# Kernel tuning notes

Hardware: AMD Instinct MI355X
Metric: run time of the kernel (lower is better)

## Reference

```python
import jax, jax.numpy as jnp
import numpy as np

N_NODES = 50000
N_EDGES = 600000
IN_CH, HID, EMB = 128, 128, 64


def _glorot(key, shape):
    fan_in, fan_out = shape[1], shape[0]
    lim = np.sqrt(6.0 / (fan_in + fan_out))
    return jax.random.uniform(key, shape, jnp.float32, -lim, lim)


def setup_inputs() -> dict:
    key = jax.random.key(0)
    ks = jax.random.split(key, 12)
    x = jax.random.normal(ks[0], (N_NODES, IN_CH), jnp.float32)
    edge_index = jax.random.randint(ks[1], (2, N_EDGES), 0, N_NODES, jnp.int64)
    return {
        "x": x,
        "edge_index": edge_index,
        # SAGEConv layer 1: lin_l (neighbor, with bias) + lin_r (root, no bias)
        "w1n": _glorot(ks[2], (HID, IN_CH)),
        "w1r": _glorot(ks[3], (HID, IN_CH)),
        "b1": jnp.zeros((HID,), jnp.float32),
        "w2n": _glorot(ks[4], (HID, HID)),
        "w2r": _glorot(ks[5], (HID, HID)),
        "b2": jnp.zeros((HID,), jnp.float32),
        "w3n": _glorot(ks[6], (EMB, HID)),
        "w3r": _glorot(ks[7], (EMB, HID)),
        "b3": jnp.zeros((EMB,), jnp.float32),
    }


def _sage_conv(x, src, dst, wn, wr, b):
    # mean aggregation of source-node features at destination nodes
    msg = x[src]                                            # [E, d_in]
    agg = jax.ops.segment_sum(msg, dst, num_segments=N_NODES)
    deg = jax.ops.segment_sum(jnp.ones((src.shape[0],), x.dtype), dst,
                              num_segments=N_NODES)
    agg = agg / jnp.maximum(deg, 1.0)[:, None]
    return agg @ wn.T + x @ wr.T + b


def reference(x, edge_index, w1n, w1r, b1, w2n, w2r, b2, w3n, w3r, b3):
    src, dst = edge_index[0], edge_index[1]
    h = jax.nn.relu(_sage_conv(x, src, dst, w1n, w1r, b1))
    # dropout(p=0.3) is identity in inference mode
    h = jax.nn.relu(_sage_conv(h, src, dst, w2n, w2r, b2))
    h = _sage_conv(h, src, dst, w3n, w3r, b3)
    return h
```

## Files before the change

### kernel.cpp

```cpp
#include <hip/hip_runtime.h>
#include <hip/hip_bf16.h>

#define NN 50000
#define ELLW 64
#define F8MINDEG 6

#define NB 128
#define BSH 9
#define BCAP 8192
#define EPB 2048

typedef short bf16x8 __attribute__((ext_vector_type(8)));
typedef float f32x4 __attribute__((ext_vector_type(4)));
typedef float floatx2 __attribute__((ext_vector_type(2)));

#if __has_builtin(__builtin_amdgcn_cvt_pk_f32_fp8) && __has_builtin(__builtin_amdgcn_cvt_pk_fp8_f32)
#define HWF8 1
#endif

__device__ __forceinline__ float bf_lo(unsigned int p) {
    union { unsigned int u; float f; } c; c.u = p << 16; return c.f;
}
__device__ __forceinline__ float bf_hi(unsigned int p) {
    union { unsigned int u; float f; } c; c.u = p & 0xffff0000u; return c.f;
}
__device__ __forceinline__ unsigned short bfbits(float f) {
    __hip_bfloat16 h = __float2bfloat16(f);
    union { __hip_bfloat16 b; unsigned short s; } c; c.b = h; return c.s;
}
__device__ __forceinline__ unsigned int pack_bf(float a, float b) {
    return (unsigned int)bfbits(a) | ((unsigned int)bfbits(b) << 16);
}
__device__ __forceinline__ void stv(float* p, float v) { *p = v; }
__device__ __forceinline__ void stv(unsigned short* p, float v) { *p = bfbits(v); }

__device__ __forceinline__ floatx2 bfpair(unsigned int p) {
    union { unsigned int u; float f; } lo, hi;
    lo.u = p << 16; hi.u = p & 0xffff0000u;
    return floatx2{lo.f, hi.f};
}
__device__ __forceinline__ void acc8v(const uint4& u, floatx2* a) {
    a[0] += bfpair(u.x); a[1] += bfpair(u.y);
    a[2] += bfpair(u.z); a[3] += bfpair(u.w);
}

__device__ __forceinline__ unsigned int enc1(float f) {
#ifdef HWF8
    return (unsigned int)__builtin_amdgcn_cvt_pk_fp8_f32(f, f, 0, false) & 0xffu;
#else
    union { float f; unsigned u; } c; c.f = f;
    unsigned s = (c.u >> 24) & 0x80u;
    float af = fabsf(f);
    if (af >= 448.f) return s | 0x7eu;
    if (af < 0.0078125f) {
        unsigned m = (unsigned)(af * 512.f + 0.5f);
        return s | (m > 7u ? 7u : m);
    }
    unsigned u = c.u & 0x7fffffffu;
    u += 0x7ffffu + ((u >> 20) & 1u);
    int e = (int)(u >> 23) - 120;
    if (e < 1) { unsigned m = (unsigned)(af * 512.f + 0.5f); return s | (m > 7u ? 7u : m); }
    if (e > 15) return s | 0x7eu;
    return s | ((unsigned)e << 3) | ((u >> 20) & 7u);
#endif
}
__device__ __forceinline__ unsigned int packf8_4(float x, float y, float z, float w) {
#ifdef HWF8
    int u = __builtin_amdgcn_cvt_pk_fp8_f32(x, y, 0, false);
    u = __builtin_amdgcn_cvt_pk_fp8_f32(z, w, u, true);
    return (unsigned int)u;
#else
    return enc1(x) | (enc1(y) << 8) | (enc1(z) << 16) | (enc1(w) << 24);
#endif
}
__device__ __forceinline__ void accf8v(const uint4& u, floatx2* a) {
#ifdef HWF8
    a[0] += __builtin_amdgcn_cvt_pk_f32_fp8(u.x, false);
    a[1] += __builtin_amdgcn_cvt_pk_f32_fp8(u.x, true);
    a[2] += __builtin_amdgcn_cvt_pk_f32_fp8(u.y, false);
    a[3] += __builtin_amdgcn_cvt_pk_f32_fp8(u.y, true);
    a[4] += __builtin_amdgcn_cvt_pk_f32_fp8(u.z, false);
    a[5] += __builtin_amdgcn_cvt_pk_f32_fp8(u.z, true);
    a[6] += __builtin_amdgcn_cvt_pk_f32_fp8(u.w, false);
    a[7] += __builtin_amdgcn_cvt_pk_f32_fp8(u.w, true);
#else
    const unsigned ww[4] = {u.x, u.y, u.z, u.w};
#pragma unroll
    for (int k = 0; k < 4; k++) {
#pragma unroll
        for (int j = 0; j < 4; j++) {
            unsigned b = (ww[k] >> (8 * j)) & 0xffu;
            unsigned v = ((b & 0x80u) << 24) | (((b & 0x7fu) + (120u << 3)) << 20);
            if ((b & 0x78u) == 0) v = 0u;
            union { unsigned u; float f; } c; c.u = v;
            a[(k * 4 + j) >> 1][(k * 4 + j) & 1] += c.f;
        }
    }
#endif
}

__global__ __launch_bounds__(256) void wb3z_kernel(
    const float* __restrict__ w1n, const float* __restrict__ w1r,
    const float* __restrict__ w2n, const float* __restrict__ w2r,
    const float* __restrict__ w3n, const float* __restrict__ w3r,
    unsigned short* __restrict__ wB1, unsigned short* __restrict__ wB2,
    unsigned short* __restrict__ wB3, unsigned int* __restrict__ bpos) {
    int i = blockIdx.x * blockDim.x + threadIdx.x;
    if (i < NB) bpos[i] = 0u;
    if (i >= 12288) return;
    if (i < 8192) {
        const float* wn = (i < 4096) ? w1n : w2n;
        const float* wr = (i < 4096) ? w1r : w2r;
        unsigned short* wB = (i < 4096) ? wB1 : wB2;
        int li = i & 4095;
        int row = li >> 5;
        int j = (li & 31) * 4;
        float4 a = *(const float4*)(wn + (size_t)row * 128 + j);
        float4 b = *(const float4*)(wr + (size_t)row * 128 + j);
        *(uint2*)(wB + (size_t)row * 256 + j) = uint2{pack_bf(a.x, a.y), pack_bf(a.z, a.w)};
        *(uint2*)(wB + (size_t)row * 256 + 128 + j) = uint2{pack_bf(b.x, b.y), pack_bf(b.z, b.w)};
    } else {
        int li = i - 8192;
        const float* w = (li < 2048) ? w3n : w3r;
        int rbase = (li < 2048) ? 0 : 64;
        int lj = li & 2047;
        int row = lj >> 5;
        int j = (lj & 31) * 4;
        float4 a = *(const float4*)(w + (size_t)row * 128 + j);
        *(uint2*)(wB3 + (size_t)(rbase + row) * 128 + j) =
            uint2{pack_bf(a.x, a.y), pack_bf(a.z, a.w)};
    }
}

__global__ __launch_bounds__(256) void binify_cvt_kernel(
    const float* __restrict__ x,
    unsigned short* __restrict__ xb,
    unsigned char* __restrict__ xf8,
    const int* __restrict__ src,
    const int* __restrict__ dst,
    unsigned int* __restrict__ bpos,
    unsigned int* __restrict__ barr,
    int n4, int E, int nEB) {
    __shared__ int cnt[NB];
    __shared__ int gbase[NB];
    const int t = threadIdx.x;
    const int blk = blockIdx.x;
    if (blk < nEB) {
        int e0 = blk * EPB;
        int ss[8], dd[8], rr[8];
        bool v[8];
#pragma unroll
        for (int k = 0; k < 8; k++) {
            int e = e0 + t + (k << 8);
            v[k] = (e < E);
            ss[k] = v[k] ? src[e] : 0;
            dd[k] = v[k] ? dst[e] : 0;
            rr[k] = 0;
        }
        if (t < NB) cnt[t] = 0;
        __syncthreads();
#pragma unroll
        for (int k = 0; k < 8; k++)
            if (v[k]) rr[k] = atomicAdd(&cnt[dd[k] >> BSH], 1);
        __syncthreads();
        if (t < NB) {
            int c = cnt[t];
            gbase[t] = c ? (int)atomicAdd(&bpos[t], (unsigned)c) : 0;
        }
        __syncthreads();
#pragma unroll
        for (int k = 0; k < 8; k++) {
            if (v[k]) {
                int b = dd[k] >> BSH;
                int pos = gbase[b] + rr[k];
                if (pos < BCAP)
                    barr[b * BCAP + pos] =
                        (unsigned)ss[k] | ((unsigned)dd[k] << 16);
            }
        }
    }
    int gtid = blk * 256 + t;
    int gs = gridDim.x << 8;
    for (int i = gtid; i < n4; i += gs) {
        float4 vv = *(const float4*)(x + 4 * (size_t)i);
        *(uint2*)(xb + 4 * (size_t)i) = uint2{pack_bf(vv.x, vv.y), pack_bf(vv.z, vv.w)};
        *(unsigned int*)(xf8 + 4 * (size_t)i) = packf8_4(vv.x, vv.y, vv.z, vv.w);
    }
}

__global__ __launch_bounds__(256) void ellbuild_kernel(
    const unsigned int* __restrict__ bpos,
    const unsigned int* __restrict__ barr,
    unsigned short* __restrict__ ell,
    int* __restrict__ cnt) {
    __shared__ alignas(16) unsigned short lell[512 * 64];
    __shared__ int lcnt[512];
    const int t = threadIdx.x;
    const int b = blockIdx.x;
    for (int i = t; i < 4096; i += 256) ((uint4*)lell)[i] = uint4{0u, 0u, 0u, 0u};
    for (int i = t; i < 512; i += 256) lcnt[i] = 0;
    __syncthreads();
    int ne = (int)bpos[b];
    if (ne > BCAP) ne = BCAP;
    const unsigned int* seg = barr + (size_t)b * BCAP;
    for (int i = t; i < ne; i += 256) {
        unsigned p = seg[i];
        int ln = (p >> 16) & 511;
        int r = atomicAdd(&lcnt[ln], 1);
        lell[(ln << 6) + (r & (ELLW - 1))] = (unsigned short)(p & 0xffffu);
    }
    __syncthreads();
    int node0 = b << BSH;
    int nn = NN - node0;
    if (nn > 512) nn = 512;
    if (nn <= 0) return;
    uint4* gell = (uint4*)(ell + (size_t)node0 * ELLW);
    const uint4* sell = (const uint4*)lell;
    for (int i = t; i < nn * 8; i += 256) gell[i] = sell[i];
    for (int i = t; i < nn; i += 256) cnt[node0 + i] = lcnt[i];
}

__global__ __launch_bounds__(256) void gather_kernel(
    const int* __restrict__ cnt, const unsigned short* __restrict__ ell,
    const unsigned char* __restrict__ hf8,
    const unsigned short* __restrict__ hb,
    unsigned short* __restrict__ axc,
    int n_nodes) {
    int tid = blockIdx.x * blockDim.x + threadIdx.x;
    int n = tid >> 3;
    if (n >= n_nodes) return;
    int c = (tid & 7) << 4;
    int deg = cnt[n];
    int dd = min(deg, ELLW);
    const unsigned short* cl = ell + (size_t)n * ELLW;
    floatx2 a[8];
#pragma unroll
    for (int k = 0; k < 8; k++) a[k] = floatx2{0.f, 0.f};
    if (deg >= F8MINDEG) {
        int i = 0;
        for (; i + 7 < dd; i += 8) {
            uint4 idv = *(const uint4*)(cl + i);
            int i0 = idv.x & 0xffff, i1 = idv.x >> 16;
            int i2 = idv.y & 0xffff, i3 = idv.y >> 16;
            int i4 = idv.z & 0xffff, i5 = idv.z >> 16;
            int i6 = idv.w & 0xffff, i7 = idv.w >> 16;
            uint4 u0 = *(const uint4*)(hf8 + (size_t)i0 * 128 + c);
            uint4 u1 = *(const uint4*)(hf8 + (size_t)i1 * 128 + c);
            uint4 u2 = *(const uint4*)(hf8 + (size_t)i2 * 128 + c);
            uint4 u3 = *(const uint4*)(hf8 + (size_t)i3 * 128 + c);
            uint4 u4 = *(const uint4*)(hf8 + (size_t)i4 * 128 + c);
            uint4 u5 = *(const uint4*)(hf8 + (size_t)i5 * 128 + c);
            uint4 u6 = *(const uint4*)(hf8 + (size_t)i6 * 128 + c);
            uint4 u7 = *(const uint4*)(hf8 + (size_t)i7 * 128 + c);
            accf8v(u0, a); accf8v(u1, a); accf8v(u2, a); accf8v(u3, a);
            accf8v(u4, a); accf8v(u5, a); accf8v(u6, a); accf8v(u7, a);
        }
        for (; i < dd; i++) {
            uint4 u = *(const uint4*)(hf8 + (size_t)cl[i] * 128 + c);
            accf8v(u, a);
        }
    } else {
        for (int i = 0; i < dd; i++) {
            int s = cl[i];
            uint4 lo = *(const uint4*)(hb + (size_t)s * 128 + c);
            uint4 hi = *(const uint4*)(hb + (size_t)s * 128 + c + 8);
            acc8v(lo, a); acc8v(hi, a + 4);
        }
    }
    float s = 1.0f / (float)max(deg, 1);
    uint4 p0 = {pack_bf(a[0][0] * s, a[0][1] * s), pack_bf(a[1][0] * s, a[1][1] * s),
                pack_bf(a[2][0] * s, a[2][1] * s), pack_bf(a[3][0] * s, a[3][1] * s)};
    uint4 p1 = {pack_bf(a[4][0] * s, a[4][1] * s), pack_bf(a[5][0] * s, a[5][1] * s),
                pack_bf(a[6][0] * s, a[6][1] * s), pack_bf(a[7][0] * s, a[7][1] * s)};
    *(uint4*)(axc + (size_t)n * 128 + c) = p0;
    *(uint4*)(axc + (size_t)n * 128 + c + 8) = p1;
}

__global__ __launch_bounds__(256) void gather_add_kernel(
    const int* __restrict__ cnt, const unsigned short* __restrict__ ell,
    const unsigned short* __restrict__ tu,
    const float* __restrict__ b3,
    float* __restrict__ out, int n_nodes) {
    int tid = blockIdx.x * blockDim.x + threadIdx.x;
    int n = tid >> 3;
    if (n >= n_nodes) return;
    int c = (tid & 7) << 3;
    int deg = cnt[n];
    int dd = min(deg, ELLW);
    const unsigned short* cl = ell + (size_t)n * ELLW;
    floatx2 a[4];
#pragma unroll
    for (int k = 0; k < 4; k++) a[k] = floatx2{0.f, 0.f};
    int i = 0;
    for (; i + 7 < dd; i += 8) {
        uint4 idv = *(const uint4*)(cl + i);
        int i0 = idv.x & 0xffff, i1 = idv.x >> 16;
        int i2 = idv.y & 0xffff, i3 = idv.y >> 16;
        int i4 = idv.z & 0xffff, i5 = idv.z >> 16;
        int i6 = idv.w & 0xffff, i7 = idv.w >> 16;
        uint4 u0 = *(const uint4*)(tu + (size_t)i0 * 128 + c);
        uint4 u1 = *(const uint4*)(tu + (size_t)i1 * 128 + c);
        uint4 u2 = *(const uint4*)(tu + (size_t)i2 * 128 + c);
        uint4 u3 = *(const uint4*)(tu + (size_t)i3 * 128 + c);
        uint4 u4 = *(const uint4*)(tu + (size_t)i4 * 128 + c);
        uint4 u5 = *(const uint4*)(tu + (size_t)i5 * 128 + c);
        uint4 u6 = *(const uint4*)(tu + (size_t)i6 * 128 + c);
        uint4 u7 = *(const uint4*)(tu + (size_t)i7 * 128 + c);
        acc8v(u0, a); acc8v(u1, a); acc8v(u2, a); acc8v(u3, a);
        acc8v(u4, a); acc8v(u5, a); acc8v(u6, a); acc8v(u7, a);
    }
    for (; i < dd; i++) {
        uint4 u = *(const uint4*)(tu + (size_t)cl[i] * 128 + c);
        acc8v(u, a);
    }
    float s = 1.0f / (float)max(deg, 1);
    uint4 uu = *(const uint4*)(tu + (size_t)n * 128 + 64 + c);
    float4 bA = *(const float4*)(b3 + c);
    float4 bB = *(const float4*)(b3 + c + 4);
    float* o = out + (size_t)n * 64 + c;
    o[0] = a[0][0] * s + bf_lo(uu.x) + bA.x;
    o[1] = a[0][1] * s + bf_hi(uu.x) + bA.y;
    o[2] = a[1][0] * s + bf_lo(uu.y) + bA.z;
    o[3] = a[1][1] * s + bf_hi(uu.y) + bA.w;
    o[4] = a[2][0] * s + bf_lo(uu.z) + bB.x;
    o[5] = a[2][1] * s + bf_hi(uu.z) + bB.y;
    o[6] = a[3][0] * s + bf_lo(uu.w) + bB.z;
    o[7] = a[3][1] * s + bf_hi(uu.w) + bB.w;
}

template <int NKS, bool RELU, bool BIAS, bool F8, typename OUT_T>
__global__ __launch_bounds__(256) void mfma_gemm(
    const unsigned short* __restrict__ A0, const unsigned short* __restrict__ A1,
    const unsigned short* __restrict__ B,
    const float* __restrict__ bias,
    OUT_T* __restrict__ out, unsigned char* __restrict__ f8out,
    int M, int N, int nTilesN) {
    constexpr int KTOT = NKS * 64;
    constexpr int LDB = KTOT + 8;
    __shared__ unsigned short As[2][128 * 72];
    __shared__ unsigned short Bs[64 * LDB];
    const int t = threadIdx.x;
    const int w = t >> 6, l = t & 63;
    const int tileM = blockIdx.x / nTilesN;
    const int n0 = (blockIdx.x - tileM * nTilesN) * 64;
    const int m0 = tileM * 128;
    const int lr = l & 15, lq = l >> 4;

    for (int c = t; c < 64 * (KTOT / 8); c += 256) {
        int row = c / (KTOT / 8);
        int ko = (c - row * (KTOT / 8)) * 8;
        *(uint4*)(&Bs[row * LDB + ko]) =
            *(const uint4*)(&B[(size_t)(n0 + row) * KTOT + ko]);
    }
    for (int c = t; c < 1024; c += 256) {
        int row = c >> 3;
        int ko = (c & 7) * 8;
        int gm = m0 + row;
        uint4 v = {0u, 0u, 0u, 0u};
        if (gm < M) v = *(const uint4*)(A0 + (size_t)gm * 128 + ko);
        *(uint4*)(&As[0][row * 72 + ko]) = v;
    }
    __syncthreads();

    f32x4 acc[2][4];
#pragma unroll
    for (int tm = 0; tm < 2; tm++)
#pragma unroll
        for (int tn = 0; tn < 4; tn++) acc[tm][tn] = f32x4{0.f, 0.f, 0.f, 0.f};

#pragma unroll
    for (int ks = 0; ks < NKS; ks++) {
        uint4 pf[4];
        if (ks + 1 < NKS) {
            int ns = ks + 1;
            const unsigned short* Asrc = (ns < NKS / 2)
                ? (A0 + (size_t)ns * 64) : (A1 + (size_t)(ns - NKS / 2) * 64);
#pragma unroll
            for (int j = 0; j < 4; j++) {
                int c = t + j * 256;
                int row = c >> 3;
                int ko = (c & 7) * 8;
                int gm = m0 + row;
                pf[j] = uint4{0u, 0u, 0u, 0u};
                if (gm < M) pf[j] = *(const uint4*)(Asrc + (size_t)gm * 128 + ko);
            }
        }
        const unsigned short* as = As[ks & 1];
#pragma unroll
        for (int kc = 0; kc < 2; kc++) {
            int lk = kc * 32 + lq * 8;
            bf16x8 af[2], bfr[4];
            af[0] = *(const bf16x8*)(&as[(w * 32 + lr) * 72 + lk]);
            af[1] = *(const bf16x8*)(&as[(w * 32 + 16 + lr) * 72 + lk]);
#pragma unroll
            for (int tn = 0; tn < 4; tn++)
                bfr[tn] = *(const bf16x8*)(&Bs[(tn * 16 + lr) * LDB + ks * 64 + lk]);
#pragma unroll
            for (int tm = 0; tm < 2; tm++)
#pragma unroll
                for (int tn = 0; tn < 4; tn++)
                    acc[tm][tn] = __builtin_amdgcn_mfma_f32_16x16x32_bf16(
                        af[tm], bfr[tn], acc[tm][tn], 0, 0, 0);
        }
        if (ks + 1 < NKS) {
#pragma unroll
            for (int j = 0; j < 4; j++) {
                int c = t + j * 256;
                int row = c >> 3;
                int ko = (c & 7) * 8;
                *(uint4*)(&As[(ks + 1) & 1][row * 72 + ko]) = pf[j];
            }
            __syncthreads();
        }
    }

#pragma unroll
    for (int tn = 0; tn < 4; tn++) {
        int n = n0 + tn * 16 + lr;
        float bj = BIAS ? bias[n] : 0.f;
#pragma unroll
        for (int tm = 0; tm < 2; tm++) {
#pragma unroll
            for (int i = 0; i < 4; i++) {
                int m = m0 + w * 32 + tm * 16 + lq * 4 + i;
                if (m < M) {
                    float v = acc[tm][tn][i] + bj;
                    if (RELU) v = fmaxf(v, 0.f);
                    stv(&out[(size_t)m * N + n], v);
                    if (F8) f8out[(size_t)m * N + n] = (unsigned char)enc1(v);
                }
            }
        }
    }
}

extern "C" void kernel_launch(void* const* d_in, const int* in_sizes, int n_in,
                              void* d_out, int out_size, void* d_ws, size_t ws_size,
                              hipStream_t stream) {
    const float* x  = (const float*)d_in[0];
    const int* ei   = (const int*)d_in[1];
    const float* w1n = (const float*)d_in[2];
    const float* w1r = (const float*)d_in[3];
    const float* b1  = (const float*)d_in[4];
    const float* w2n = (const float*)d_in[5];
    const float* w2r = (const float*)d_in[6];
    const float* b2  = (const float*)d_in[7];
    const float* w3n = (const float*)d_in[8];
    const float* w3r = (const float*)d_in[9];
    const float* b3  = (const float*)d_in[10];
    float* out = (float*)d_out;

    const int E = in_sizes[1] / 2;
    const int* src = ei;
    const int* dst = ei + E;

    char* ws = (char*)d_ws;
    unsigned short* xb  = (unsigned short*)(ws);
    unsigned short* axc = (unsigned short*)(ws + 12800000);
    unsigned short* h1b = (unsigned short*)(ws + 25600000);
    unsigned short* h2b = (unsigned short*)(ws + 38400000);
    unsigned int* barr  = (unsigned int*)(ws + 38400000);
    int* cnt            = (int*)  (ws + 51200000);
    unsigned int* bpos  = (unsigned int*)(ws + 51400192);
    unsigned short* ell = (unsigned short*)(ws + 54400000);
    unsigned short* wB1 = (unsigned short*)(ws + 60800000);
    unsigned short* wB2 = (unsigned short*)(ws + 60865536);
    unsigned short* wB3 = (unsigned short*)(ws + 60931072);
    unsigned char* xf8  = (unsigned char*)(ws + 60963840);
    unsigned char* h1f8 = (unsigned char*)(ws + 67363840);

    const int nEB = (E + EPB - 1) / EPB;

    wb3z_kernel<<<48, 256, 0, stream>>>(
        w1n, w1r, w2n, w2r, w3n, w3r, wB1, wB2, wB3, bpos);
    binify_cvt_kernel<<<2048, 256, 0, stream>>>(x, xb, xf8, src, dst,
                                                bpos, barr, NN * 32, E, nEB);
    ellbuild_kernel<<<(NN + 511) / 512, 256, 0, stream>>>(bpos, barr, ell, cnt);

    const int gatherBlocks = (NN * 8 + 255) / 256;
    const int mTiles = (NN + 127) / 128;

    gather_kernel<<<gatherBlocks, 256, 0, stream>>>(cnt, ell, xf8, xb, axc, NN);
    mfma_gemm<4, true, true, true, unsigned short>
        <<<mTiles * 2, 256, 0, stream>>>(axc, xb, wB1, b1, h1b, h1f8, NN, 128, 2);

    gather_kernel<<<gatherBlocks, 256, 0, stream>>>(cnt, ell, h1f8, h1b, axc, NN);
    mfma_gemm<4, true, true, false, unsigned short>
        <<<mTiles * 2, 256, 0, stream>>>(axc, h1b, wB2, b2, h2b, nullptr, NN, 128, 2);

    mfma_gemm<2, false, false, false, unsigned short>
        <<<mTiles * 2, 256, 0, stream>>>(h2b, h2b + 64, wB3, nullptr, axc, nullptr,
                                         NN, 128, 2);
    gather_add_kernel<<<gatherBlocks, 256, 0, stream>>>(
        cnt, ell, axc, b3, out, NN);
}
```

Measured before the change: 233.5 us.

## Sort nodes by degree and pad ELL rows with zero-row sentinel

Builds a degree histogram in the ELL build, prefix-sums it, and scatters nodes into a degree-sorted ELL copy with a permutation. The gathers then iterate in that sorted order, so neighbouring threads have similar degrees and wavefront divergence drops. ELL padding now points at a zeroed sentinel row, which removes the scalar tail loops and lets every iteration fetch eight neighbours at once. This adds two small kernels and an extra pass that copies the ELL, and it spends bandwidth loading padding entries.

Result: slower. 337.4 us (+44.5%).

```diff
diff --git a/kernel.cpp b/kernel.cpp
--- a/kernel.cpp
+++ b/kernel.cpp
@@ -2,6 +2,7 @@
 #include <hip/hip_bf16.h>
 
 #define NN 50000
+#define ZROW 50000
 #define ELLW 64
 #define F8MINDEG 6
 
@@ -104,9 +105,20 @@
     const float* __restrict__ w2n, const float* __restrict__ w2r,
     const float* __restrict__ w3n, const float* __restrict__ w3r,
     unsigned short* __restrict__ wB1, unsigned short* __restrict__ wB2,
-    unsigned short* __restrict__ wB3, unsigned int* __restrict__ bpos) {
+    unsigned short* __restrict__ wB3, int* __restrict__ zblk,
+    unsigned short* __restrict__ xb, unsigned short* __restrict__ axc,
+    unsigned short* __restrict__ h1b,
+    unsigned char* __restrict__ xf8, unsigned char* __restrict__ h1f8) {
     int i = blockIdx.x * blockDim.x + threadIdx.x;
-    if (i < NB) bpos[i] = 0u;
+    if (i < 2048) zblk[i] = 0;
+    int p = i - 2048;
+    if (p >= 0 && p < 256) {
+        if (p < 64)       ((unsigned int*)(xb  + (size_t)ZROW * 128))[p] = 0u;
+        else if (p < 128) ((unsigned int*)(axc + (size_t)ZROW * 128))[p - 64] = 0u;
+        else if (p < 192) ((unsigned int*)(h1b + (size_t)ZROW * 128))[p - 128] = 0u;
+        else if (p < 224) ((unsigned int*)(xf8 + (size_t)ZROW * 128))[p - 192] = 0u;
+        else              ((unsigned int*)(h1f8 + (size_t)ZROW * 128))[p - 224] = 0u;
+    }
     if (i >= 12288) return;
     if (i < 8192) {
         const float* wn = (i < 4096) ? w1n : w2n;
@@ -192,13 +204,17 @@
     const unsigned int* __restrict__ bpos,
     const unsigned int* __restrict__ barr,
     unsigned short* __restrict__ ell,
-    int* __restrict__ cnt) {
+    int* __restrict__ cnt,
+    int* __restrict__ hist) {
     __shared__ alignas(16) unsigned short lell[512 * 64];
     __shared__ int lcnt[512];
+    __shared__ int lh[65];
     const int t = threadIdx.x;
     const int b = blockIdx.x;
-    for (int i = t; i < 4096; i += 256) ((uint4*)lell)[i] = uint4{0u, 0u, 0u, 0u};
+    const unsigned PADP = 0xC350C350u;
+    for (int i = t; i < 4096; i += 256) ((uint4*)lell)[i] = uint4{PADP, PADP, PADP, PADP};
     for (int i = t; i < 512; i += 256) lcnt[i] = 0;
+    if (t < 65) lh[t] = 0;
     __syncthreads();
     int ne = (int)bpos[b];
     if (ne > BCAP) ne = BCAP;
@@ -217,28 +233,60 @@
     uint4* gell = (uint4*)(ell + (size_t)node0 * ELLW);
     const uint4* sell = (const uint4*)lell;
     for (int i = t; i < nn * 8; i += 256) gell[i] = sell[i];
-    for (int i = t; i < nn; i += 256) cnt[node0 + i] = lcnt[i];
+    for (int i = t; i < nn; i += 256) {
+        int d = lcnt[i];
+        cnt[node0 + i] = d;
+        atomicAdd(&lh[min(d, 64)], 1);
+    }
+    __syncthreads();
+    if (t < 65 && lh[t]) atomicAdd(&hist[t], lh[t]);
+}
+
+__global__ void prefix65_kernel(const int* __restrict__ hist, int* __restrict__ cursor) {
+    if (threadIdx.x == 0) {
+        int r = 0;
+        for (int d = 0; d <= 64; d++) { cursor[d * 16] = r; r += hist[d]; }
+    }
+}
+
+__global__ __launch_bounds__(256) void place_kernel(
+    const int* __restrict__ cnt, int* __restrict__ cursor,
+    const unsigned short* __restrict__ ell,
+    unsigned short* __restrict__ ell2,
+    int* __restrict__ perm, int* __restrict__ degS) {
+    int tid = blockIdx.x * blockDim.x + threadIdx.x;
+    int n = tid >> 3, ln = tid & 7;
+    if (n >= NN) return;
+    int deg = cnt[n];
+    int pos = 0;
+    if (ln == 0) pos = atomicAdd(&cursor[min(deg, 64) * 16], 1);
+    int lane = threadIdx.x & 63;
+    pos = __shfl(pos, lane & 56, 64);
+    ((uint4*)(ell2 + (size_t)pos * ELLW))[ln] =
+        ((const uint4*)(ell + (size_t)n * ELLW))[ln];
+    if (ln == 0) { perm[pos] = n; degS[pos] = deg; }
 }
 
 __global__ __launch_bounds__(256) void gather_kernel(
-    const int* __restrict__ cnt, const unsigned short* __restrict__ ell,
+    const int* __restrict__ degS, const int* __restrict__ perm,
+    const unsigned short* __restrict__ ell2,
     const unsigned char* __restrict__ hf8,
     const unsigned short* __restrict__ hb,
     unsigned short* __restrict__ axc,
     int n_nodes) {
     int tid = blockIdx.x * blockDim.x + threadIdx.x;
-    int n = tid >> 3;
-    if (n >= n_nodes) return;
+    int j = tid >> 3;
+    if (j >= n_nodes) return;
     int c = (tid & 7) << 4;
-    int deg = cnt[n];
-    int dd = min(deg, ELLW);
-    const unsigned short* cl = ell + (size_t)n * ELLW;
+    int deg = degS[j];
+    int n = perm[j];
+    int dd8 = (min(deg, ELLW) + 7) & ~7;
+    const unsigned short* cl = ell2 + (size_t)j * ELLW;
     floatx2 a[8];
 #pragma unroll
     for (int k = 0; k < 8; k++) a[k] = floatx2{0.f, 0.f};
     if (deg >= F8MINDEG) {
-        int i = 0;
-        for (; i + 7 < dd; i += 8) {
+        for (int i = 0; i < dd8; i += 8) {
             uint4 idv = *(const uint4*)(cl + i);
             int i0 = idv.x & 0xffff, i1 = idv.x >> 16;
             int i2 = idv.y & 0xffff, i3 = idv.y >> 16;
@@ -255,16 +303,20 @@
             accf8v(u0, a); accf8v(u1, a); accf8v(u2, a); accf8v(u3, a);
             accf8v(u4, a); accf8v(u5, a); accf8v(u6, a); accf8v(u7, a);
         }
-        for (; i < dd; i++) {
-            uint4 u = *(const uint4*)(hf8 + (size_t)cl[i] * 128 + c);
-            accf8v(u, a);
-        }
     } else {
-        for (int i = 0; i < dd; i++) {
-            int s = cl[i];
-            uint4 lo = *(const uint4*)(hb + (size_t)s * 128 + c);
-            uint4 hi = *(const uint4*)(hb + (size_t)s * 128 + c + 8);
-            acc8v(lo, a); acc8v(hi, a + 4);
+        for (int i = 0; i < dd8; i += 8) {
+            uint4 idv = *(const uint4*)(cl + i);
+            int is[8];
+            is[0] = idv.x & 0xffff; is[1] = idv.x >> 16;
+            is[2] = idv.y & 0xffff; is[3] = idv.y >> 16;
+            is[4] = idv.z & 0xffff; is[5] = idv.z >> 16;
+            is[6] = idv.w & 0xffff; is[7] = idv.w >> 16;
+#pragma unroll
+            for (int k = 0; k < 8; k++) {
+                uint4 lo = *(const uint4*)(hb + (size_t)is[k] * 128 + c);
+                uint4 hi = *(const uint4*)(hb + (size_t)is[k] * 128 + c + 8);
+                acc8v(lo, a); acc8v(hi, a + 4);
+            }
         }
     }
     float s = 1.0f / (float)max(deg, 1);
@@ -277,22 +329,23 @@
 }
 
 __global__ __launch_bounds__(256) void gather_add_kernel(
-    const int* __restrict__ cnt, const unsigned short* __restrict__ ell,
+    const int* __restrict__ degS, const int* __restrict__ perm,
+    const unsigned short* __restrict__ ell2,
     const unsigned short* __restrict__ tu,
     const float* __restrict__ b3,
     float* __restrict__ out, int n_nodes) {
     int tid = blockIdx.x * blockDim.x + threadIdx.x;
-    int n = tid >> 3;
-    if (n >= n_nodes) return;
+    int j = tid >> 3;
+    if (j >= n_nodes) return;
     int c = (tid & 7) << 3;
-    int deg = cnt[n];
-    int dd = min(deg, ELLW);
-    const unsigned short* cl = ell + (size_t)n * ELLW;
+    int deg = degS[j];
+    int n = perm[j];
+    int dd8 = (min(deg, ELLW) + 7) & ~7;
+    const unsigned short* cl = ell2 + (size_t)j * ELLW;
     floatx2 a[4];
 #pragma unroll
     for (int k = 0; k < 4; k++) a[k] = floatx2{0.f, 0.f};
-    int i = 0;
-    for (; i + 7 < dd; i += 8) {
+    for (int i = 0; i < dd8; i += 8) {
         uint4 idv = *(const uint4*)(cl + i);
         int i0 = idv.x & 0xffff, i1 = idv.x >> 16;
         int i2 = idv.y & 0xffff, i3 = idv.y >> 16;
@@ -308,10 +361,6 @@
         uint4 u7 = *(const uint4*)(tu + (size_t)i7 * 128 + c);
         acc8v(u0, a); acc8v(u1, a); acc8v(u2, a); acc8v(u3, a);
         acc8v(u4, a); acc8v(u5, a); acc8v(u6, a); acc8v(u7, a);
-    }
-    for (; i < dd; i++) {
-        uint4 u = *(const uint4*)(tu + (size_t)cl[i] * 128 + c);
-        acc8v(u, a);
     }
     float s = 1.0f / (float)max(deg, 1);
     uint4 uu = *(const uint4*)(tu + (size_t)n * 128 + 64 + c);
@@ -456,35 +505,44 @@
 
     char* ws = (char*)d_ws;
     unsigned short* xb  = (unsigned short*)(ws);
-    unsigned short* axc = (unsigned short*)(ws + 12800000);
-    unsigned short* h1b = (unsigned short*)(ws + 25600000);
-    unsigned short* h2b = (unsigned short*)(ws + 38400000);
-    unsigned int* barr  = (unsigned int*)(ws + 38400000);
-    int* cnt            = (int*)  (ws + 51200000);
-    unsigned int* bpos  = (unsigned int*)(ws + 51400192);
-    unsigned short* ell = (unsigned short*)(ws + 54400000);
-    unsigned short* wB1 = (unsigned short*)(ws + 60800000);
-    unsigned short* wB2 = (unsigned short*)(ws + 60865536);
-    unsigned short* wB3 = (unsigned short*)(ws + 60931072);
-    unsigned char* xf8  = (unsigned char*)(ws + 60963840);
-    unsigned char* h1f8 = (unsigned char*)(ws + 67363840);
+    unsigned short* axc = (unsigned short*)(ws + 13000000);
+    unsigned short* h1b = (unsigned short*)(ws + 26000000);
+    unsigned short* h2b = (unsigned short*)(ws + 39000000);
+    unsigned int* barr  = (unsigned int*)(ws + 39000000);
+    unsigned short* ell = (unsigned short*)(ws + 52000000);
+    unsigned short* ell2= (unsigned short*)(ws + 58400000);
+    int* cnt            = (int*)  (ws + 64800000);
+    int* perm           = (int*)  (ws + 65000000);
+    int* degS           = (int*)  (ws + 65200000);
+    int* zblk           = (int*)  (ws + 65400000);
+    int* hist           = zblk;
+    int* cursor         = zblk + 256;
+    unsigned int* bpos  = (unsigned int*)(zblk + 1536);
+    unsigned short* wB1 = (unsigned short*)(ws + 65500000);
+    unsigned short* wB2 = (unsigned short*)(ws + 65600000);
+    unsigned short* wB3 = (unsigned short*)(ws + 65700000);
+    unsigned char* xf8  = (unsigned char*)(ws + 65800000);
+    unsigned char* h1f8 = (unsigned char*)(ws + 72300000);
 
     const int nEB = (E + EPB - 1) / EPB;
 
     wb3z_kernel<<<48, 256, 0, stream>>>(
-        w1n, w1r, w2n, w2r, w3n, w3r, wB1, wB2, wB3, bpos);
+        w1n, w1r, w2n, w2r, w3n, w3r, wB1, wB2, wB3, zblk, xb, axc, h1b, xf8, h1f8);
     binify_cvt_kernel<<<2048, 256, 0, stream>>>(x, xb, xf8, src, dst,
                                                 bpos, barr, NN * 32, E, nEB);
-    ellbuild_kernel<<<(NN + 511) / 512, 256, 0, stream>>>(bpos, barr, ell, cnt);
+    ellbuild_kernel<<<(NN + 511) / 512, 256, 0, stream>>>(bpos, barr, ell, cnt, hist);
+    prefix65_kernel<<<1, 64, 0, stream>>>(hist, cursor);
+    place_kernel<<<(NN * 8 + 255) / 256, 256, 0, stream>>>(cnt, cursor, ell, ell2,
+                                                           perm, degS);
 
     const int gatherBlocks = (NN * 8 + 255) / 256;
     const int mTiles = (NN + 127) / 128;
 
-    gather_kernel<<<gatherBlocks, 256, 0, stream>>>(cnt, ell, xf8, xb, axc, NN);
+    gather_kernel<<<gatherBlocks, 256, 0, stream>>>(degS, perm, ell2, xf8, xb, axc, NN);
     mfma_gemm<4, true, true, true, unsigned short>
         <<<mTiles * 2, 256, 0, stream>>>(axc, xb, wB1, b1, h1b, h1f8, NN, 128, 2);
 
-    gather_kernel<<<gatherBlocks, 256, 0, stream>>>(cnt, ell, h1f8, h1b, axc, NN);
+    gather_kernel<<<gatherBlocks, 256, 0, stream>>>(degS, perm, ell2, h1f8, h1b, axc, NN);
     mfma_gemm<4, true, true, false, unsigned short>
         <<<mTiles * 2, 256, 0, stream>>>(axc, h1b, wB2, b2, h2b, nullptr, NN, 128, 2);
 
@@ -492,5 +550,5 @@
         <<<mTiles * 2, 256, 0, stream>>>(h2b, h2b + 64, wB3, nullptr, axc, nullptr,
                                          NN, 128, 2);
     gather_add_kernel<<<gatherBlocks, 256, 0, stream>>>(
-        cnt, ell, axc, b3, out, NN);
-}
+        degS, perm, ell2, axc, b3, out, NN);
+}
```
